# Performance work log

Measured on AMD Instinct MI355X. Metric: run time of the kernel, lower is better.

Reference implementation:

```python
import jax, jax.numpy as jnp
import numpy as np

B, N, E, H = 16, 577, 1024, 16          # batch, tokens (1 cls + 24x24 patches), embed, heads
HD = E // H
LORA_E, LORA_R = 4, 16                   # LoRA experts, rank
AD_E, AD_D = 4, 64                       # adapter experts, bottleneck
FF = 4 * E


def setup_inputs() -> dict:
    key = jax.random.key(0)
    ks = jax.random.split(key, 12)
    p = lambda i, shape: jax.random.normal(ks[i], shape, dtype=jnp.float32) * 0.02
    return {
        "tokens": jax.random.normal(ks[0], (B, N, E), dtype=jnp.float32),
        "ln1_g": jnp.ones((E,), jnp.float32), "ln1_b": jnp.zeros((E,), jnp.float32),
        "qkv_w": p(1, (3 * E, E)), "qkv_b": jnp.zeros((3 * E,), jnp.float32),
        "proj_w": p(2, (E, E)), "proj_b": jnp.zeros((E,), jnp.float32),
        "lora_gate_w": p(3, (LORA_E, E)),
        "lora_A": p(4, (LORA_E, LORA_R, E)),
        "lora_B": p(5, (LORA_E, 3 * E, LORA_R)),
        "ln2_g": jnp.ones((E,), jnp.float32), "ln2_b": jnp.zeros((E,), jnp.float32),
        "fc1_w": p(6, (FF, E)), "fc1_b": jnp.zeros((FF,), jnp.float32),
        "fc2_w": p(7, (E, FF)), "fc2_b": jnp.zeros((E,), jnp.float32),
        "ad_gate_w": p(8, (AD_E, E)),
        "ad_down_w": p(9, (AD_E, AD_D, E)), "ad_down_b": jnp.zeros((AD_E, AD_D), jnp.float32),
        "ad_up_w": p(10, (AD_E, E, AD_D)), "ad_up_b": jnp.zeros((AD_E, E), jnp.float32),
    }


def _ln(x, g, b):
    m = x.mean(-1, keepdims=True)
    v = ((x - m) ** 2).mean(-1, keepdims=True)
    return (x - m) * jax.lax.rsqrt(v + 1e-6) * g + b


def reference(tokens, ln1_g, ln1_b, qkv_w, qkv_b, proj_w, proj_b,
              lora_gate_w, lora_A, lora_B, ln2_g, ln2_b,
              fc1_w, fc1_b, fc2_w, fc2_b,
              ad_gate_w, ad_down_w, ad_down_b, ad_up_w, ad_up_b):
    # ---- attention with MoE-LoRA delta on fused QKV ----
    normed = _ln(tokens, ln1_g, ln1_b)                      # [B,N,E]
    qkv = normed @ qkv_w.T + qkv_b                          # [B,N,3E]
    gates = jax.nn.softmax(normed @ lora_gate_w.T, axis=-1)  # [B,N,X]
    h = jnp.einsum('bnd,xrd->bnxr', normed, lora_A)         # low-rank down
    delta = jnp.einsum('bnxr,bnx,xor->bno', h, gates, lora_B)  # gate-weighted up
    qkv = (qkv + delta).reshape(B, N, 3, H, HD).transpose(2, 0, 3, 1, 4)
    q, k, v = qkv[0], qkv[1], qkv[2]                        # [B,H,N,hd]
    scores = jnp.einsum('bhqd,bhkd->bhqk', q, k) * (HD ** -0.5)
    probs = jax.nn.softmax(scores, axis=-1)
    ctx = jnp.einsum('bhqk,bhkd->bhqd', probs, v)
    ctx = ctx.transpose(0, 2, 1, 3).reshape(B, N, E)
    tokens = tokens + (ctx @ proj_w.T + proj_b)
    # ---- MLP + MoE adapter branch (shared norm2 input) ----
    mlp_in = _ln(tokens, ln2_g, ln2_b)
    mlp_out = jax.nn.gelu(mlp_in @ fc1_w.T + fc1_b, approximate=False) @ fc2_w.T + fc2_b
    ag = jax.nn.softmax(mlp_in @ ad_gate_w.T, axis=-1)       # [B,N,Xa]
    ah = jax.nn.gelu(jnp.einsum('bnd,xhd->bnxh', mlp_in, ad_down_w) + ad_down_b,
                     approximate=False)
    ad_out = (jnp.einsum('bnxh,bnx,xoh->bno', ah, ag, ad_up_w)
              + jnp.einsum('bnx,xo->bno', ag, ad_up_b))
    return tokens + mlp_out + ad_out
```

## Files before the change

### kernel.cpp

```cpp
#include <hip/hip_runtime.h>
#include <math.h>

#define TOK 9232
#define EMB 1024
#define NQKV 3072
#define FFD 4096
#define NSEQ 577

typedef __bf16 bf16x8 __attribute__((ext_vector_type(8)));
typedef float f32x4 __attribute__((ext_vector_type(4)));
typedef unsigned short ushort8 __attribute__((ext_vector_type(8)));
typedef unsigned short ushort4v __attribute__((ext_vector_type(4)));

typedef __attribute__((address_space(3))) unsigned int lds_u32_t;
typedef const __attribute__((address_space(1))) unsigned int glob_u32_t;

__device__ __forceinline__ void async16(void* lds, const void* g) {
    __builtin_amdgcn_global_load_lds((glob_u32_t*)g, (lds_u32_t*)lds, 16, 0, 0);
}

__device__ __forceinline__ unsigned short f2bf(float f) {
    unsigned int u = __builtin_bit_cast(unsigned int, f);
    u = (u + 0x7fffu + ((u >> 16) & 1u)) >> 16;
    return (unsigned short)u;
}
__device__ __forceinline__ float bf2f(unsigned short s) {
    unsigned int u = ((unsigned int)s) << 16;
    return __builtin_bit_cast(float, u);
}
__device__ __forceinline__ float gelu_exact(float x) {
    return 0.5f * x * (1.0f + erff(x * 0.70710678118654752f));
}

__global__ void k_pack_all(const float* __restrict__ s_qkv, const float* __restrict__ s_proj,
                           const float* __restrict__ s_fc1, const float* __restrict__ s_fc2,
                           const float* __restrict__ s_la,  const float* __restrict__ s_ad,
                           unsigned short* __restrict__ d_qkv, unsigned short* __restrict__ d_proj,
                           unsigned short* __restrict__ d_fc1, unsigned short* __restrict__ d_fc2,
                           unsigned short* __restrict__ d_la,  unsigned short* __restrict__ d_ad) {
    int stride = gridDim.x * 256;
    for (int i4 = blockIdx.x * 256 + threadIdx.x; i4 < 3227648; i4 += stride) {
        const float* s; unsigned short* d; int local;
        if (i4 < 786432)       { s = s_qkv;  d = d_qkv;  local = i4; }
        else if (i4 < 1048576) { s = s_proj; d = d_proj; local = i4 - 786432; }
        else if (i4 < 2097152) { s = s_fc1;  d = d_fc1;  local = i4 - 1048576; }
        else if (i4 < 3145728) { s = s_fc2;  d = d_fc2;  local = i4 - 2097152; }
        else if (i4 < 3162112) { s = s_la;   d = d_la;   local = i4 - 3145728; }
        else                   { s = s_ad;   d = d_ad;   local = i4 - 3162112; }
        float4 v = ((const float4*)s)[local];
        ushort4v o;
        o[0] = f2bf(v.x); o[1] = f2bf(v.y); o[2] = f2bf(v.z); o[3] = f2bf(v.w);
        ((ushort4v*)d)[local] = o;
    }
}
__global__ void k_pack_bcat(const float* __restrict__ Bw, unsigned short* __restrict__ out) {
    int i = blockIdx.x * 256 + threadIdx.x;
    if (i >= 3072 * 64) return;
    int o = i >> 6, j = i & 63, x = j >> 4, r = j & 15;
    out[o * 64 + j] = f2bf(Bw[x * 3072 * 16 + o * 16 + r]);
}
__global__ void k_pack_u(const float* __restrict__ Uw, unsigned short* __restrict__ out) {
    int i = blockIdx.x * 256 + threadIdx.x;
    if (i >= 1024 * 256) return;
    int o = i >> 8, j = i & 255, x = j >> 6, h = j & 63;
    out[o * 256 + j] = f2bf(Uw[x * 65536 + o * 64 + h]);
}

template<bool FC2I>
__global__ __launch_bounds__(256) void k_ln_gates(const float* __restrict__ x,
                                                  const float* __restrict__ g,
                                                  const float* __restrict__ b,
                                                  const float* __restrict__ gw,
                                                  unsigned short* __restrict__ out,
                                                  float* __restrict__ gates,
                                                  const float* __restrict__ fc2b,
                                                  const float* __restrict__ upb,
                                                  float* __restrict__ out2) {
    int t = blockIdx.x;
    int tid = threadIdx.x;
    const float* xp = x + (size_t)t * EMB;
    float4 v = ((const float4*)xp)[tid];
    float s = v.x + v.y + v.z + v.w;
    float sq = v.x * v.x + v.y * v.y + v.z * v.z + v.w * v.w;
    #pragma unroll
    for (int off = 32; off > 0; off >>= 1) {
        s += __shfl_down(s, off);
        sq += __shfl_down(sq, off);
    }
    __shared__ float red[8];
    if ((tid & 63) == 0) { red[tid >> 6] = s; red[(tid >> 6) + 4] = sq; }
    __syncthreads();
    float S = red[0] + red[1] + red[2] + red[3];
    float SQ = red[4] + red[5] + red[6] + red[7];
    float mean = S * (1.0f / EMB);
    float var = SQ * (1.0f / EMB) - mean * mean;
    float rstd = rsqrtf(var + 1e-6f);
    float4 gv = ((const float4*)g)[tid];
    float4 bv = ((const float4*)b)[tid];
    float n0 = (v.x - mean) * rstd * gv.x + bv.x;
    float n1 = (v.y - mean) * rstd * gv.y + bv.y;
    float n2 = (v.z - mean) * rstd * gv.z + bv.z;
    float n3 = (v.w - mean) * rstd * gv.w + bv.w;
    ushort4v o;
    o[0] = f2bf(n0); o[1] = f2bf(n1); o[2] = f2bf(n2); o[3] = f2bf(n3);
    ((ushort4v*)(out + (size_t)t * EMB))[tid] = o;
    float p[4];
    #pragma unroll
    for (int xx = 0; xx < 4; ++xx) {
        float4 gr = ((const float4*)(gw + xx * EMB))[tid];
        p[xx] = n0 * gr.x + n1 * gr.y + n2 * gr.z + n3 * gr.w;
    }
    #pragma unroll
    for (int off = 32; off > 0; off >>= 1) {
        #pragma unroll
        for (int xx = 0; xx < 4; ++xx) p[xx] += __shfl_down(p[xx], off);
    }
    __shared__ float red2[4][4];
    __shared__ float agb[4];
    if ((tid & 63) == 0) {
        #pragma unroll
        for (int xx = 0; xx < 4; ++xx) red2[tid >> 6][xx] = p[xx];
    }
    __syncthreads();
    if (tid == 0) {
        float l[4];
        #pragma unroll
        for (int xx = 0; xx < 4; ++xx) l[xx] = red2[0][xx] + red2[1][xx] + red2[2][xx] + red2[3][xx];
        float m = fmaxf(fmaxf(l[0], l[1]), fmaxf(l[2], l[3]));
        float e[4], ssum = 0.f;
        #pragma unroll
        for (int xx = 0; xx < 4; ++xx) { e[xx] = expf(l[xx] - m); ssum += e[xx]; }
        float inv = 1.0f / ssum;
        #pragma unroll
        for (int xx = 0; xx < 4; ++xx) {
            float gg = e[xx] * inv;
            gates[t * 4 + xx] = gg;
            if (FC2I) agb[xx] = gg;
        }
    }
    if (FC2I) {
        __syncthreads();
        float g0 = agb[0], g1 = agb[1], g2 = agb[2], g3 = agb[3];
        float4 b0 = ((const float4*)(upb + 0 * EMB))[tid];
        float4 b1 = ((const float4*)(upb + 1 * EMB))[tid];
        float4 b2 = ((const float4*)(upb + 2 * EMB))[tid];
        float4 b3 = ((const float4*)(upb + 3 * EMB))[tid];
        float4 fb = ((const float4*)fc2b)[tid];
        float4 r;
        r.x = v.x + fb.x + g0 * b0.x + g1 * b1.x + g2 * b2.x + g3 * b3.x;
        r.y = v.y + fb.y + g0 * b0.y + g1 * b1.y + g2 * b2.y + g3 * b3.y;
        r.z = v.z + fb.z + g0 * b0.z + g1 * b1.z + g2 * b2.z + g3 * b3.z;
        r.w = v.w + fb.w + g0 * b0.w + g1 * b1.w + g2 * b2.w + g3 * b3.w;
        ((float4*)(out2 + (size_t)t * EMB))[tid] = r;
    }
}

#define BAR __builtin_amdgcn_s_barrier()

template<bool GELU, bool BF16OUT, int GG, int MF, int NF, int CN>
__global__ __launch_bounds__(256) void k_gemm(
    const unsigned short* __restrict__ A, int lda,
    const unsigned short* __restrict__ W, int ldw, int K1,
    int M, int N,
    const unsigned short* __restrict__ A2, const unsigned short* __restrict__ W2, int K2,
    const float* __restrict__ bias, const float* __restrict__ resid,
    const float* __restrict__ aux,
    void* __restrict__ Cout, int ldc, int gy)
{
    constexpr int CA = MF * 4;
    constexpr int CB = NF * 4;
    constexpr int CT = CA + CB;
    constexpr int CPW = CT / 4;
    constexpr int BUFB = CT * 1024;
    __shared__ __attribute__((aligned(16))) char Sbuf[2 * BUFB];

    int tid = threadIdx.x;
    int nwg = gridDim.x, orig = blockIdx.x;
    int xcd = orig & 7, lid = orig >> 3;
    int q = nwg >> 3, r = nwg & 7;
    int wg = (xcd < r ? xcd * (q + 1) : r * (q + 1) + (xcd - r) * q) + lid;
    int nmt = nwg / gy;
    int ni = wg % CN;
    int tmp = wg / CN;
    int mt = tmp % nmt;
    int nt = (tmp / nmt) * CN + ni;
    int bm = mt * (MF * 32);
    int bn = nt * (NF * 32);

    int l = tid & 63, w = tid >> 6;
    int wr = w >> 1, wc = w & 1;
    int lr = l & 15;
    int sslot = (((l & 7) ^ (l >> 3)) << 3);

    int KT1 = K1 >> 6, KT2 = K2 >> 6;
    int KT = KT1 + KT2;

    const unsigned short* A2s = A2 ? A2 : A;
    const unsigned short* W2s = W2 ? W2 : W;
    int K2s = A2 ? K2 : lda;

    const unsigned short* sp1[CPW];
    const unsigned short* sp2[CPW];
    int ldsu[CPW];
    #pragma unroll
    for (int j = 0; j < CPW; ++j) {
        int c = w * CPW + j;
        ldsu[j] = c << 10;
        if (c < CA) {
            int rw = bm + c * 8 + (l >> 3); if (rw > M - 1) rw = M - 1;
            sp1[j] = A + (size_t)rw * lda + sslot;
            sp2[j] = A2s + (size_t)rw * K2s + sslot;
        } else {
            int rw = bn + (c - CA) * 8 + (l >> 3); if (rw > N - 1) rw = N - 1;
            sp1[j] = W + (size_t)rw * ldw + sslot;
            sp2[j] = W2s + (size_t)rw * K2s + sslot;
        }
    }

    int offA[MF][2], offB[NF][2];
    #pragma unroll
    for (int m = 0; m < MF; ++m)
        #pragma unroll
        for (int ks = 0; ks < 2; ++ks) {
            int rw = wr * (MF * 16) + m * 16 + lr;
            int g = ks * 4 + (l >> 4);
            offA[m][ks] = (rw << 7) + ((g ^ (rw & 7)) << 4);
        }
    #pragma unroll
    for (int n = 0; n < NF; ++n)
        #pragma unroll
        for (int ks = 0; ks < 2; ++ks) {
            int rw = wc * (NF * 16) + n * 16 + lr;
            int g = ks * 4 + (l >> 4);
            offB[n][ks] = (CA << 10) + (rw << 7) + ((g ^ (rw & 7)) << 4);
        }

    f32x4 acc[MF][NF];
    #pragma unroll
    for (int m = 0; m < MF; ++m)
        #pragma unroll
        for (int n = 0; n < NF; ++n) acc[m][n] = (f32x4){0.f, 0.f, 0.f, 0.f};

    auto stage = [&](int ss, int bb) {
        char* db = Sbuf + bb * BUFB;
        if (ss < KT1) {
            int ko = ss << 6;
            #pragma unroll
            for (int j = 0; j < CPW; ++j) async16(db + ldsu[j], sp1[j] + ko);
        } else {
            int ko = (ss - KT1) << 6;
            #pragma unroll
            for (int j = 0; j < CPW; ++j) async16(db + ldsu[j], sp2[j] + ko);
        }
    };

    stage(0, 0);

    #pragma unroll 1
    for (int t = 0; t < KT; ++t) {
        asm volatile("s_waitcnt vmcnt(0)" ::: "memory");
        BAR;
        __builtin_amdgcn_sched_barrier(0);
        int s = t + 1; if (s >= KT) s = 0;
        stage(s, (t + 1) & 1);
        const char* base = Sbuf + (t & 1) * BUFB;
        bf16x8 af[MF][2], bfr[NF][2];
        #pragma unroll
        for (int m = 0; m < MF; ++m)
            #pragma unroll
            for (int ks = 0; ks < 2; ++ks) af[m][ks] = *(const bf16x8*)(base + offA[m][ks]);
        #pragma unroll
        for (int n = 0; n < NF; ++n)
            #pragma unroll
            for (int ks = 0; ks < 2; ++ks) bfr[n][ks] = *(const bf16x8*)(base + offB[n][ks]);
        __builtin_amdgcn_s_setprio(1);
        #pragma unroll
        for (int m = 0; m < MF; ++m)
            #pragma unroll
            for (int n = 0; n < NF; ++n)
                #pragma unroll
                for (int ks = 0; ks < 2; ++ks)
                    acc[m][n] = __builtin_amdgcn_mfma_f32_16x16x32_bf16(af[m][ks], bfr[n][ks], acc[m][n], 0, 0, 0);
        __builtin_amdgcn_s_setprio(0);
    }

    int rbase = bm + wr * (MF * 16);
    int cbase = bn + wc * (NF * 16);
    #pragma unroll
    for (int n = 0; n < NF; ++n) {
        int col = cbase + n * 16 + lr;
        if (col >= N) continue;
        float bv = bias ? bias[col] : 0.0f;
        #pragma unroll
        for (int m = 0; m < MF; ++m) {
            #pragma unroll
            for (int rr = 0; rr < 4; ++rr) {
                int row = rbase + m * 16 + (l >> 4) * 4 + rr;
                if (row >= M) continue;
                float c = acc[m][n][rr] + bv;
                if (GELU) c = gelu_exact(c);
                if (GG > 0) c *= aux[row * 4 + col / (GG > 0 ? GG : 1)];
                if (resid) c += resid[(size_t)row * ldc + col];
                if (BF16OUT) ((unsigned short*)Cout)[(size_t)row * ldc + col] = f2bf(c);
                else ((float*)Cout)[(size_t)row * ldc + col] = c;
            }
        }
    }
}

__global__ __launch_bounds__(256) void k_attn(const unsigned short* __restrict__ qkv,
                                              unsigned short* __restrict__ ctx) {
    int bh = blockIdx.x;
    int qt = blockIdx.y;
    int b = bh >> 4, h = bh & 15;
    int tid = threadIdx.x;
    int l = tid & 63;
    int w = tid >> 6;
    int lr = l & 15;
    int lk = (l >> 4) * 8;

    __shared__ unsigned short Qs[64][72];
    __shared__ unsigned short Ks[64][72];
    __shared__ unsigned short Vt[64][72];
    __shared__ unsigned short Ps[64][72];

    const size_t base = (size_t)b * NSEQ * NQKV + (size_t)h * 64;
    int q0 = qt * 64;

    {
        int row = tid >> 2, ds = (tid & 3) * 16;
        int qrow = q0 + row;
        if (qrow < NSEQ) {
            const unsigned short* src = qkv + base + (size_t)qrow * NQKV + ds;
            #pragma unroll
            for (int j = 0; j < 16; ++j) Qs[row][ds + j] = f2bf(bf2f(src[j]) * 0.125f);
        } else {
            #pragma unroll
            for (int j = 0; j < 16; ++j) Qs[row][ds + j] = 0;
        }
    }

    float m_run[4], l_run[4];
    f32x4 o[4];
    #pragma unroll
    for (int r = 0; r < 4; ++r) { m_run[r] = -1e30f; l_run[r] = 0.0f; }
    #pragma unroll
    for (int n = 0; n < 4; ++n) o[n] = (f32x4){0.f, 0.f, 0.f, 0.f};

    for (int kt = 0; kt < 10; ++kt) {
        __syncthreads();
        {
            int row = tid >> 2, ds = (tid & 3) * 16;
            int key = kt * 64 + row;
            if (key < NSEQ) {
                const unsigned short* ksrc = qkv + base + (size_t)key * NQKV + 1024 + ds;
                *(ushort8*)&Ks[row][ds] = *(const ushort8*)ksrc;
                *(ushort8*)&Ks[row][ds + 8] = *(const ushort8*)(ksrc + 8);
                const unsigned short* vsrc = qkv + base + (size_t)key * NQKV + 2048 + ds;
                #pragma unroll
                for (int j = 0; j < 16; ++j) Vt[ds + j][row] = vsrc[j];
            } else {
                ushort8 z = {};
                *(ushort8*)&Ks[row][ds] = z;
                *(ushort8*)&Ks[row][ds + 8] = z;
                #pragma unroll
                for (int j = 0; j < 16; ++j) Vt[ds + j][row] = 0;
            }
        }
        __syncthreads();

        f32x4 s[4];
        #pragma unroll
        for (int n = 0; n < 4; ++n) s[n] = (f32x4){0.f, 0.f, 0.f, 0.f};
        #pragma unroll
        for (int ks = 0; ks < 2; ++ks) {
            bf16x8 qa = *(const bf16x8*)&Qs[w * 16 + lr][ks * 32 + lk];
            #pragma unroll
            for (int n = 0; n < 4; ++n) {
                bf16x8 kb = *(const bf16x8*)&Ks[n * 16 + lr][ks * 32 + lk];
                s[n] = __builtin_amdgcn_mfma_f32_16x16x32_bf16(qa, kb, s[n], 0, 0, 0);
            }
        }
        #pragma unroll
        for (int n = 0; n < 4; ++n) {
            int col = kt * 64 + n * 16 + lr;
            if (col >= NSEQ) {
                #pragma unroll
                for (int r = 0; r < 4; ++r) s[n][r] = -1e30f;
            }
        }
        float tmax[4];
        #pragma unroll
        for (int r = 0; r < 4; ++r)
            tmax[r] = fmaxf(fmaxf(s[0][r], s[1][r]), fmaxf(s[2][r], s[3][r]));
        #pragma unroll
        for (int off = 1; off < 16; off <<= 1) {
            #pragma unroll
            for (int r = 0; r < 4; ++r) tmax[r] = fmaxf(tmax[r], __shfl_xor(tmax[r], off));
        }
        float alpha[4], rs[4];
        #pragma unroll
        for (int r = 0; r < 4; ++r) {
            float mn = fmaxf(m_run[r], tmax[r]);
            alpha[r] = __expf(m_run[r] - mn);
            m_run[r] = mn;
            rs[r] = 0.0f;
        }
        #pragma unroll
        for (int n = 0; n < 4; ++n) {
            #pragma unroll
            for (int r = 0; r < 4; ++r) {
                float p = __expf(s[n][r] - m_run[r]);
                s[n][r] = p;
                rs[r] += p;
            }
        }
        #pragma unroll
        for (int off = 1; off < 16; off <<= 1) {
            #pragma unroll
            for (int r = 0; r < 4; ++r) rs[r] += __shfl_xor(rs[r], off);
        }
        #pragma unroll
        for (int r = 0; r < 4; ++r) l_run[r] = l_run[r] * alpha[r] + rs[r];
        #pragma unroll
        for (int n = 0; n < 4; ++n) {
            #pragma unroll
            for (int r = 0; r < 4; ++r) o[n][r] *= alpha[r];
        }
        #pragma unroll
        for (int n = 0; n < 4; ++n) {
            #pragma unroll
            for (int r = 0; r < 4; ++r)
                Ps[w * 16 + (l >> 4) * 4 + r][n * 16 + lr] = f2bf(s[n][r]);
        }
        __syncthreads();
        #pragma unroll
        for (int ks = 0; ks < 2; ++ks) {
            bf16x8 pa = *(const bf16x8*)&Ps[w * 16 + lr][ks * 32 + lk];
            #pragma unroll
            for (int n = 0; n < 4; ++n) {
                bf16x8 vb = *(const bf16x8*)&Vt[n * 16 + lr][ks * 32 + lk];
                o[n] = __builtin_amdgcn_mfma_f32_16x16x32_bf16(pa, vb, o[n], 0, 0, 0);
            }
        }
    }
    #pragma unroll
    for (int r = 0; r < 4; ++r) {
        int qrow = q0 + w * 16 + (l >> 4) * 4 + r;
        if (qrow < NSEQ) {
            float inv = (l_run[r] > 0.f) ? 1.0f / l_run[r] : 0.0f;
            #pragma unroll
            for (int n = 0; n < 4; ++n)
                ctx[((size_t)b * NSEQ + qrow) * EMB + h * 64 + n * 16 + lr] = f2bf(o[n][r] * inv);
        }
    }
}

extern "C" void kernel_launch(void* const* d_in, const int* in_sizes, int n_in,
                              void* d_out, int out_size, void* d_ws, size_t ws_size,
                              hipStream_t stream) {
    const float* tokens      = (const float*)d_in[0];
    const float* ln1_g       = (const float*)d_in[1];
    const float* ln1_b       = (const float*)d_in[2];
    const float* qkv_w       = (const float*)d_in[3];
    const float* qkv_b       = (const float*)d_in[4];
    const float* proj_w      = (const float*)d_in[5];
    const float* proj_b      = (const float*)d_in[6];
    const float* lora_gate_w = (const float*)d_in[7];
    const float* lora_A      = (const float*)d_in[8];
    const float* lora_B      = (const float*)d_in[9];
    const float* ln2_g       = (const float*)d_in[10];
    const float* ln2_b       = (const float*)d_in[11];
    const float* fc1_w       = (const float*)d_in[12];
    const float* fc1_b       = (const float*)d_in[13];
    const float* fc2_w       = (const float*)d_in[14];
    const float* fc2_b       = (const float*)d_in[15];
    const float* ad_gate_w   = (const float*)d_in[16];
    const float* ad_down_w   = (const float*)d_in[17];
    const float* ad_down_b   = (const float*)d_in[18];
    const float* ad_up_w     = (const float*)d_in[19];
    const float* ad_up_b     = (const float*)d_in[20];

    char* ws = (char*)d_ws;
    size_t off = 0;
    auto alloc = [&](size_t bytes) -> void* {
        void* p = ws + off;
        off += (bytes + 255) & ~(size_t)255;
        return p;
    };

    unsigned short* w_qkv  = (unsigned short*)alloc((size_t)NQKV * EMB * 2);
    unsigned short* w_proj = (unsigned short*)alloc((size_t)EMB * EMB * 2);
    unsigned short* w_fc1  = (unsigned short*)alloc((size_t)FFD * EMB * 2);
    unsigned short* w_fc2  = (unsigned short*)alloc((size_t)EMB * FFD * 2);
    unsigned short* w_acat = (unsigned short*)alloc((size_t)64 * EMB * 2);
    unsigned short* w_bcat = (unsigned short*)alloc((size_t)NQKV * 64 * 2);
    unsigned short* w_dcat = (unsigned short*)alloc((size_t)256 * EMB * 2);
    unsigned short* w_u    = (unsigned short*)alloc((size_t)EMB * 256 * 2);

    unsigned short* u1 = (unsigned short*)alloc((size_t)TOK * EMB * 2);
    unsigned short* u2 = (unsigned short*)alloc((size_t)TOK * EMB * 2);
    unsigned short* u3 = (unsigned short*)alloc((size_t)TOK * FFD * 2);
    float* tok2  = (float*)alloc((size_t)TOK * EMB * 4);
    unsigned short* hw  = (unsigned short*)alloc((size_t)TOK * 64 * 2);
    unsigned short* ahw = (unsigned short*)alloc((size_t)TOK * 256 * 2);
    float* gates = (float*)alloc((size_t)TOK * 4 * 4);
    float* ag    = (float*)alloc((size_t)TOK * 4 * 4);

    unsigned short* normed = u1;
    unsigned short* mlpin  = u1;
    unsigned short* ctx    = u2;
    unsigned short* qkv    = u3;
    unsigned short* h1     = u3;

    k_pack_all<<<2048, 256, 0, stream>>>(qkv_w, proj_w, fc1_w, fc2_w, lora_A, ad_down_w,
                                         w_qkv, w_proj, w_fc1, w_fc2, w_acat, w_dcat);
    k_pack_bcat<<<(NQKV * 64 + 255) / 256, 256, 0, stream>>>(lora_B, w_bcat);
    k_pack_u<<<(EMB * 256 + 255) / 256, 256, 0, stream>>>(ad_up_w, w_u);

    k_ln_gates<false><<<TOK, 256, 0, stream>>>(tokens, ln1_g, ln1_b, lora_gate_w,
                                               normed, gates, nullptr, nullptr, nullptr);
    k_gemm<false, true, 16, 2, 2, 1><<<145, 256, 0, stream>>>(
        normed, EMB, w_acat, EMB, EMB, TOK, 64,
        nullptr, nullptr, 0, nullptr, nullptr, gates, hw, 64, 1);
    k_gemm<false, true, 0, 4, 2, 8><<<73 * 48, 256, 0, stream>>>(
        normed, EMB, w_qkv, EMB, EMB, TOK, NQKV,
        hw, w_bcat, 64, qkv_b, nullptr, nullptr, qkv, NQKV, 48);
    k_attn<<<dim3(256, 10), 256, 0, stream>>>(qkv, ctx);
    k_gemm<false, false, 0, 2, 2, 8><<<145 * 16, 256, 0, stream>>>(
        ctx, EMB, w_proj, EMB, EMB, TOK, EMB,
        nullptr, nullptr, 0, proj_b, tokens, nullptr, tok2, EMB, 16);
    k_ln_gates<true><<<TOK, 256, 0, stream>>>(tok2, ln2_g, ln2_b, ad_gate_w,
                                              mlpin, ag, fc2_b, ad_up_b, (float*)d_out);
    k_gemm<true, true, 64, 2, 2, 4><<<145 * 4, 256, 0, stream>>>(
        mlpin, EMB, w_dcat, EMB, EMB, TOK, 256,
        nullptr, nullptr, 0, ad_down_b, nullptr, ag, ahw, 256, 4);
    k_gemm<true, true, 0, 4, 2, 8><<<73 * 64, 256, 0, stream>>>(
        mlpin, EMB, w_fc1, EMB, EMB, TOK, FFD,
        nullptr, nullptr, 0, fc1_b, nullptr, nullptr, h1, FFD, 64);
    k_gemm<false, false, 0, 4, 2, 8><<<73 * 16, 256, 0, stream>>>(
        h1, FFD, w_fc2, FFD, FFD, TOK, EMB,
        ahw, w_u, 256, nullptr, (const float*)d_out, nullptr, (float*)d_out, EMB, 16);
}
```

Baseline: 633.3 us.

## Fuse adapter down-projection into fc1 GEMM and concatenate fc2 with adapter up

The adapter down-projection weights are appended to fc1 as extra output columns (N=4352). Gate scaling is applied in the epilogue for those columns, and fc2's weights are concatenated with the adapter-up weights so the final GEMM uses a single K=4352 loop. This removes a separate small GEMM launch and the dual-source K loop. It also changes the proj GEMM tile config and moves the Q scaling from the load path to the scores. The costs are extra weight-packing launches and a larger intermediate buffer.

```diff
diff --git a/kernel.cpp b/kernel.cpp
--- a/kernel.cpp
+++ b/kernel.cpp
@@ -5,6 +5,7 @@
 #define EMB 1024
 #define NQKV 3072
 #define FFD 4096
+#define FF2 4352
 #define NSEQ 577
 
 typedef __bf16 bf16x8 __attribute__((ext_vector_type(8)));
@@ -33,25 +34,39 @@
 }
 
 __global__ void k_pack_all(const float* __restrict__ s_qkv, const float* __restrict__ s_proj,
-                           const float* __restrict__ s_fc1, const float* __restrict__ s_fc2,
-                           const float* __restrict__ s_la,  const float* __restrict__ s_ad,
+                           const float* __restrict__ s_fc1, const float* __restrict__ s_la,
+                           const float* __restrict__ s_ad,
                            unsigned short* __restrict__ d_qkv, unsigned short* __restrict__ d_proj,
-                           unsigned short* __restrict__ d_fc1, unsigned short* __restrict__ d_fc2,
-                           unsigned short* __restrict__ d_la,  unsigned short* __restrict__ d_ad) {
+                           unsigned short* __restrict__ d_fc1, unsigned short* __restrict__ d_la,
+                           unsigned short* __restrict__ d_ad) {
     int stride = gridDim.x * 256;
-    for (int i4 = blockIdx.x * 256 + threadIdx.x; i4 < 3227648; i4 += stride) {
+    for (int i4 = blockIdx.x * 256 + threadIdx.x; i4 < 2179072; i4 += stride) {
         const float* s; unsigned short* d; int local;
         if (i4 < 786432)       { s = s_qkv;  d = d_qkv;  local = i4; }
         else if (i4 < 1048576) { s = s_proj; d = d_proj; local = i4 - 786432; }
         else if (i4 < 2097152) { s = s_fc1;  d = d_fc1;  local = i4 - 1048576; }
-        else if (i4 < 3145728) { s = s_fc2;  d = d_fc2;  local = i4 - 2097152; }
-        else if (i4 < 3162112) { s = s_la;   d = d_la;   local = i4 - 3145728; }
-        else                   { s = s_ad;   d = d_ad;   local = i4 - 3162112; }
+        else if (i4 < 2113536) { s = s_la;   d = d_la;   local = i4 - 2097152; }
+        else                   { s = s_ad;   d = d_ad;   local = i4 - 2113536; }
         float4 v = ((const float4*)s)[local];
         ushort4v o;
         o[0] = f2bf(v.x); o[1] = f2bf(v.y); o[2] = f2bf(v.z); o[3] = f2bf(v.w);
         ((ushort4v*)d)[local] = o;
     }
+}
+__global__ void k_pack_fc2cat(const float* __restrict__ src, unsigned short* __restrict__ dst) {
+    int i = blockIdx.x * 256 + threadIdx.x;
+    if (i >= 1024 * 1024) return;
+    int o = i >> 10, c4 = i & 1023;
+    float4 v = ((const float4*)src)[i];
+    ushort4v q;
+    q[0] = f2bf(v.x); q[1] = f2bf(v.y); q[2] = f2bf(v.z); q[3] = f2bf(v.w);
+    *(ushort4v*)(dst + (size_t)o * FF2 + c4 * 4) = q;
+}
+__global__ void k_pack_u(const float* __restrict__ Uw, unsigned short* __restrict__ out) {
+    int i = blockIdx.x * 256 + threadIdx.x;
+    if (i >= 1024 * 256) return;
+    int o = i >> 8, j = i & 255, x = j >> 6, h = j & 63;
+    out[(size_t)o * FF2 + 4096 + j] = f2bf(Uw[x * 65536 + o * 64 + h]);
 }
 __global__ void k_pack_bcat(const float* __restrict__ Bw, unsigned short* __restrict__ out) {
     int i = blockIdx.x * 256 + threadIdx.x;
@@ -59,11 +74,11 @@
     int o = i >> 6, j = i & 63, x = j >> 4, r = j & 15;
     out[o * 64 + j] = f2bf(Bw[x * 3072 * 16 + o * 16 + r]);
 }
-__global__ void k_pack_u(const float* __restrict__ Uw, unsigned short* __restrict__ out) {
+__global__ void k_pack_bias(const float* __restrict__ b1, const float* __restrict__ b2,
+                            float* __restrict__ out) {
     int i = blockIdx.x * 256 + threadIdx.x;
-    if (i >= 1024 * 256) return;
-    int o = i >> 8, j = i & 255, x = j >> 6, h = j & 63;
-    out[o * 256 + j] = f2bf(Uw[x * 65536 + o * 64 + h]);
+    if (i >= FF2) return;
+    out[i] = (i < 4096) ? b1[i] : b2[i - 4096];
 }
 
 template<bool FC2I>
@@ -157,7 +172,7 @@
 
 #define BAR __builtin_amdgcn_s_barrier()
 
-template<bool GELU, bool BF16OUT, int GG, int MF, int NF, int CN>
+template<bool GELU, bool BF16OUT, int GG, bool AD, int NSPLIT, int MF, int NF, int CN>
 __global__ __launch_bounds__(256) void k_gemm(
     const unsigned short* __restrict__ A, int lda,
     const unsigned short* __restrict__ W, int ldw, int K1,
@@ -196,7 +211,6 @@
     int KT = KT1 + KT2;
 
     const unsigned short* A2s = A2 ? A2 : A;
-    const unsigned short* W2s = W2 ? W2 : W;
     int K2s = A2 ? K2 : lda;
 
     const unsigned short* sp1[CPW];
@@ -212,8 +226,12 @@
             sp2[j] = A2s + (size_t)rw * K2s + sslot;
         } else {
             int rw = bn + (c - CA) * 8 + (l >> 3); if (rw > N - 1) rw = N - 1;
-            sp1[j] = W + (size_t)rw * ldw + sslot;
-            sp2[j] = W2s + (size_t)rw * K2s + sslot;
+            const unsigned short* wp;
+            if (NSPLIT > 0 && rw >= NSPLIT) wp = W2 + (size_t)(rw - NSPLIT) * ldw + sslot;
+            else                            wp = W + (size_t)rw * ldw + sslot;
+            sp1[j] = wp;
+            sp2[j] = (NSPLIT > 0) ? wp
+                     : ((A2 ? W2 : W) + (size_t)rw * K2s + sslot);
         }
     }
 
@@ -300,6 +318,7 @@
                 float c = acc[m][n][rr] + bv;
                 if (GELU) c = gelu_exact(c);
                 if (GG > 0) c *= aux[row * 4 + col / (GG > 0 ? GG : 1)];
+                if (AD) { if (col >= 4096) c *= aux[row * 4 + ((col - 4096) >> 6)]; }
                 if (resid) c += resid[(size_t)row * ldc + col];
                 if (BF16OUT) ((unsigned short*)Cout)[(size_t)row * ldc + col] = f2bf(c);
                 else ((float*)Cout)[(size_t)row * ldc + col] = c;
@@ -332,11 +351,12 @@
         int qrow = q0 + row;
         if (qrow < NSEQ) {
             const unsigned short* src = qkv + base + (size_t)qrow * NQKV + ds;
-            #pragma unroll
-            for (int j = 0; j < 16; ++j) Qs[row][ds + j] = f2bf(bf2f(src[j]) * 0.125f);
+            *(ushort8*)&Qs[row][ds] = *(const ushort8*)src;
+            *(ushort8*)&Qs[row][ds + 8] = *(const ushort8*)(src + 8);
         } else {
-            #pragma unroll
-            for (int j = 0; j < 16; ++j) Qs[row][ds + j] = 0;
+            ushort8 z = {};
+            *(ushort8*)&Qs[row][ds] = z;
+            *(ushort8*)&Qs[row][ds + 8] = z;
         }
     }
 
@@ -380,6 +400,11 @@
                 bf16x8 kb = *(const bf16x8*)&Ks[n * 16 + lr][ks * 32 + lk];
                 s[n] = __builtin_amdgcn_mfma_f32_16x16x32_bf16(qa, kb, s[n], 0, 0, 0);
             }
+        }
+        #pragma unroll
+        for (int n = 0; n < 4; ++n) {
+            #pragma unroll
+            for (int r = 0; r < 4; ++r) s[n][r] *= 0.125f;
         }
         #pragma unroll
         for (int n = 0; n < 4; ++n) {
@@ -489,21 +514,20 @@
         return p;
     };
 
-    unsigned short* w_qkv  = (unsigned short*)alloc((size_t)NQKV * EMB * 2);
-    unsigned short* w_proj = (unsigned short*)alloc((size_t)EMB * EMB * 2);
-    unsigned short* w_fc1  = (unsigned short*)alloc((size_t)FFD * EMB * 2);
-    unsigned short* w_fc2  = (unsigned short*)alloc((size_t)EMB * FFD * 2);
-    unsigned short* w_acat = (unsigned short*)alloc((size_t)64 * EMB * 2);
-    unsigned short* w_bcat = (unsigned short*)alloc((size_t)NQKV * 64 * 2);
-    unsigned short* w_dcat = (unsigned short*)alloc((size_t)256 * EMB * 2);
-    unsigned short* w_u    = (unsigned short*)alloc((size_t)EMB * 256 * 2);
+    unsigned short* w_qkv    = (unsigned short*)alloc((size_t)NQKV * EMB * 2);
+    unsigned short* w_proj   = (unsigned short*)alloc((size_t)EMB * EMB * 2);
+    unsigned short* w_fc1    = (unsigned short*)alloc((size_t)FFD * EMB * 2);
+    unsigned short* w_fc2cat = (unsigned short*)alloc((size_t)EMB * FF2 * 2);
+    unsigned short* w_acat   = (unsigned short*)alloc((size_t)64 * EMB * 2);
+    unsigned short* w_bcat   = (unsigned short*)alloc((size_t)NQKV * 64 * 2);
+    unsigned short* w_dcat   = (unsigned short*)alloc((size_t)256 * EMB * 2);
+    float* b_fc1cat = (float*)alloc((size_t)FF2 * 4);
 
     unsigned short* u1 = (unsigned short*)alloc((size_t)TOK * EMB * 2);
     unsigned short* u2 = (unsigned short*)alloc((size_t)TOK * EMB * 2);
-    unsigned short* u3 = (unsigned short*)alloc((size_t)TOK * FFD * 2);
+    unsigned short* u3 = (unsigned short*)alloc((size_t)TOK * FF2 * 2);
     float* tok2  = (float*)alloc((size_t)TOK * EMB * 4);
     unsigned short* hw  = (unsigned short*)alloc((size_t)TOK * 64 * 2);
-    unsigned short* ahw = (unsigned short*)alloc((size_t)TOK * 256 * 2);
     float* gates = (float*)alloc((size_t)TOK * 4 * 4);
     float* ag    = (float*)alloc((size_t)TOK * 4 * 4);
 
@@ -511,34 +535,33 @@
     unsigned short* mlpin  = u1;
     unsigned short* ctx    = u2;
     unsigned short* qkv    = u3;
-    unsigned short* h1     = u3;
-
-    k_pack_all<<<2048, 256, 0, stream>>>(qkv_w, proj_w, fc1_w, fc2_w, lora_A, ad_down_w,
-                                         w_qkv, w_proj, w_fc1, w_fc2, w_acat, w_dcat);
+    unsigned short* h1cat  = u3;
+
+    k_pack_all<<<2048, 256, 0, stream>>>(qkv_w, proj_w, fc1_w, lora_A, ad_down_w,
+                                         w_qkv, w_proj, w_fc1, w_acat, w_dcat);
+    k_pack_fc2cat<<<(1024 * 1024 + 255) / 256, 256, 0, stream>>>(fc2_w, w_fc2cat);
+    k_pack_u<<<(EMB * 256 + 255) / 256, 256, 0, stream>>>(ad_up_w, w_fc2cat);
     k_pack_bcat<<<(NQKV * 64 + 255) / 256, 256, 0, stream>>>(lora_B, w_bcat);
-    k_pack_u<<<(EMB * 256 + 255) / 256, 256, 0, stream>>>(ad_up_w, w_u);
+    k_pack_bias<<<(FF2 + 255) / 256, 256, 0, stream>>>(fc1_b, ad_down_b, b_fc1cat);
 
     k_ln_gates<false><<<TOK, 256, 0, stream>>>(tokens, ln1_g, ln1_b, lora_gate_w,
                                                normed, gates, nullptr, nullptr, nullptr);
-    k_gemm<false, true, 16, 2, 2, 1><<<145, 256, 0, stream>>>(
+    k_gemm<false, true, 16, false, 0, 2, 2, 1><<<145, 256, 0, stream>>>(
         normed, EMB, w_acat, EMB, EMB, TOK, 64,
         nullptr, nullptr, 0, nullptr, nullptr, gates, hw, 64, 1);
-    k_gemm<false, true, 0, 4, 2, 8><<<73 * 48, 256, 0, stream>>>(
+    k_gemm<false, true, 0, false, 0, 4, 2, 8><<<73 * 48, 256, 0, stream>>>(
         normed, EMB, w_qkv, EMB, EMB, TOK, NQKV,
         hw, w_bcat, 64, qkv_b, nullptr, nullptr, qkv, NQKV, 48);
     k_attn<<<dim3(256, 10), 256, 0, stream>>>(qkv, ctx);
-    k_gemm<false, false, 0, 2, 2, 8><<<145 * 16, 256, 0, stream>>>(
+    k_gemm<false, false, 0, false, 0, 4, 2, 8><<<73 * 16, 256, 0, stream>>>(
         ctx, EMB, w_proj, EMB, EMB, TOK, EMB,
         nullptr, nullptr, 0, proj_b, tokens, nullptr, tok2, EMB, 16);
     k_ln_gates<true><<<TOK, 256, 0, stream>>>(tok2, ln2_g, ln2_b, ad_gate_w,
                                               mlpin, ag, fc2_b, ad_up_b, (float*)d_out);
-    k_gemm<true, true, 64, 2, 2, 4><<<145 * 4, 256, 0, stream>>>(
-        mlpin, EMB, w_dcat, EMB, EMB, TOK, 256,
-        nullptr, nullptr, 0, ad_down_b, nullptr, ag, ahw, 256, 4);
-    k_gemm<true, true, 0, 4, 2, 8><<<73 * 64, 256, 0, stream>>>(
-        mlpin, EMB, w_fc1, EMB, EMB, TOK, FFD,
-        nullptr, nullptr, 0, fc1_b, nullptr, nullptr, h1, FFD, 64);
-    k_gemm<false, false, 0, 4, 2, 8><<<73 * 16, 256, 0, stream>>>(
-        h1, FFD, w_fc2, FFD, FFD, TOK, EMB,
-        ahw, w_u, 256, nullptr, (const float*)d_out, nullptr, (float*)d_out, EMB, 16);
-}
+    k_gemm<true, true, 0, true, 4096, 4, 2, 4><<<73 * 68, 256, 0, stream>>>(
+        mlpin, EMB, w_fc1, EMB, EMB, TOK, FF2,
+        nullptr, w_dcat, 0, b_fc1cat, nullptr, ag, h1cat, FF2, 68);
+    k_gemm<false, false, 0, false, 0, 4, 2, 8><<<73 * 16, 256, 0, stream>>>(
+        h1cat, FF2, w_fc2cat, FF2, FF2, TOK, EMB,
+        nullptr, nullptr, 0, nullptr, (const float*)d_out, nullptr, (float*)d_out, EMB, 16);
+}
```

After: 651.1 us. 2.8% more time.
